# Optimization experiments

Measured on AMD Instinct MI355X. Metric: run time of the kernel, lower is better.

The kernel has to match this reference:

```python
import jax, jax.numpy as jnp
import numpy as np

N = 500_000   # total nodes across the batch of session graphs
B = 8192      # number of graphs
D = 128       # input_dim == output_dim (fc_out is None)
H = 128       # hidden_dim


def setup_inputs() -> dict:
    key = jax.random.key(0)
    ks = jax.random.split(key, 7)
    x_invar = jax.random.normal(ks[0], (N, D), jnp.float32)
    x_var = jax.random.normal(ks[1], (N, D), jnp.float32)
    s = 1.0 / np.sqrt(D)
    Wu = jax.random.normal(ks[2], (H, D), jnp.float32) * s
    bu = jnp.zeros((H,), jnp.float32)
    Wv = jax.random.normal(ks[3], (H, D), jnp.float32) * s
    We = jax.random.normal(ks[4], (1, H), jnp.float32) * (1.0 / np.sqrt(H))
    # sorted segment ids; guarantee every graph has >= 1 node
    seg_ids = jnp.sort(jnp.concatenate([
        jnp.arange(B, dtype=jnp.int32),
        jax.random.randint(ks[5], (N - B,), 0, B, dtype=jnp.int32),
    ]))
    # last node index of each graph = cumsum(counts) - 1
    counts = jax.ops.segment_sum(jnp.ones((N,), jnp.int32), seg_ids, num_segments=B)
    last_nodes = (jnp.cumsum(counts) - 1).astype(jnp.int32)
    return dict(x_invar=x_invar, x_var=x_var, Wu=Wu, bu=bu, Wv=Wv, We=We,
                seg_ids=seg_ids, last_nodes=last_nodes, num_graphs=B)


def _segment_softmax(e, seg, num_segments):
    # e: [M]; numerically stable per-segment softmax
    m = jax.ops.segment_max(e, seg, num_segments=num_segments)
    ex = jnp.exp(e - m[seg])
    den = jax.ops.segment_sum(ex, seg, num_segments=num_segments)
    return ex / den[seg]


def reference(x_invar, x_var, Wu, bu, Wv, We, seg_ids, last_nodes, num_graphs):
    # hybrid granularity, order=1: per-graph [invar; var] node rows.
    # Segment softmax/sum are permutation-invariant within a segment, so we
    # concatenate globally and double the segment ids.
    feats = jnp.concatenate([x_invar, x_var], axis=0)          # [2N, D]
    seg2 = jnp.concatenate([seg_ids, seg_ids], axis=0)         # [2N]
    feat_u = feats @ Wu.T + bu                                 # [2N, H]
    v_invar = (x_invar[last_nodes] @ Wv.T)[seg2]               # [2N, H]
    v_var = (x_var[last_nodes] @ Wv.T)[seg2]                   # [2N, H]
    e_invar = (jax.nn.sigmoid(feat_u + v_invar) @ We.T)[:, 0]  # [2N]
    e_var = (jax.nn.sigmoid(feat_u + v_var) @ We.T)[:, 0]      # [2N]
    a_invar = _segment_softmax(e_invar, seg2, num_graphs)[:, None]
    a_var = _segment_softmax(e_var, seg2, num_graphs)[:, None]
    rst_invar = jax.ops.segment_sum(feats * a_invar, seg2, num_segments=num_graphs)  # [B, D]
    rst_var = jax.ops.segment_sum(feats * a_var, seg2, num_segments=num_graphs)      # [B, D]
    return rst_invar[:, None, :], rst_var[:, None, :]          # [B, 1, D] each (order=1)
```

## Files before the change

kernel.cpp:

```cpp
#include <hip/hip_runtime.h>
#include <stdint.h>

typedef short short8 __attribute__((ext_vector_type(8)));
typedef float f32x4 __attribute__((ext_vector_type(4)));

#define D 128
#define LOG2E 1.44269504088896340736f

__device__ __forceinline__ unsigned short f2bf(float f) {
    union { float f; unsigned u; } v; v.f = f;
    unsigned u = v.u;
    unsigned r = (u + 0x7FFFu + ((u >> 16) & 1u)) >> 16;
    return (unsigned short)r;
}

__device__ __forceinline__ unsigned packbf(float x, float y) {
    unsigned ux = __float_as_uint(x) + 0x8000u;
    unsigned uy = __float_as_uint(y) + 0x8000u;
    return __builtin_amdgcn_perm(uy, ux, 0x07060302u);
}

__device__ __forceinline__ float sigm2(float z) {
    return __builtin_amdgcn_rcpf(1.f + __builtin_amdgcn_exp2f(-z));
}

__device__ __forceinline__ void gld16(const float* g, float* l) {
    __builtin_amdgcn_global_load_lds(
        (const __attribute__((address_space(1))) void*)g,
        (__attribute__((address_space(3))) void*)l, 16, 0, 0);
}

__global__ __launch_bounds__(256) void pack_wu(const float* __restrict__ Wu,
                                               short8* __restrict__ frag) {
    int tid = blockIdx.x * 256 + threadIdx.x;
    int nt = tid >> 8, kk = (tid >> 6) & 3, l = tid & 63;
    int col = nt * 16 + (l & 15);
    int kb  = kk * 32 + ((l >> 4) * 8);
    short8 o;
#pragma unroll
    for (int j = 0; j < 8; ++j) o[j] = (short)f2bf(Wu[col * D + kb + j] * LOG2E);
    frag[tid] = o;
}

__global__ __launch_bounds__(128) void gate_k(const float* __restrict__ xI,
                                              const float* __restrict__ xV,
                                              const float* __restrict__ Wv,
                                              const float* __restrict__ bu,
                                              const int* __restrict__ lastn,
                                              float* __restrict__ vIb,
                                              float* __restrict__ vVb) {
    __shared__ float xi[D], xv[D];
    int g = blockIdx.x, t = threadIdx.x;
    int r = lastn[g];
    xi[t] = xI[(size_t)r * D + t];
    xv[t] = xV[(size_t)r * D + t];
    __syncthreads();
    const float4* wr = (const float4*)(Wv + (size_t)t * D);
    const float4* a4 = (const float4*)xi;
    const float4* b4 = (const float4*)xv;
    float sI = 0.f, sV = 0.f;
#pragma unroll 8
    for (int i = 0; i < D / 4; ++i) {
        float4 w = wr[i], a = a4[i], b = b4[i];
        sI += w.x * a.x + w.y * a.y + w.z * a.z + w.w * a.w;
        sV += w.x * b.x + w.y * b.y + w.z * b.z + w.w * b.w;
    }
    float bias = bu[t];
    vIb[(size_t)g * D + t] = (sI + bias) * LOG2E;
    vVb[(size_t)g * D + t] = (sV + bias) * LOG2E;
}

__global__ __launch_bounds__(256) void attn_main(
    const float* __restrict__ xI, const float* __restrict__ xV,
    const float* __restrict__ We, const int* __restrict__ lastn,
    const float* __restrict__ vIb, const float* __restrict__ vVb,
    const short8* __restrict__ fragG, float* __restrict__ out, int B) {
    __shared__ short8 bfrag[2048];
    __shared__ __align__(16) float rbuf[4][2048];
    __shared__ float gl[3][D];
    __shared__ float cmbA[2][4][D];
    __shared__ float cmbM[2][4], cmbL[2][4];

    int t = threadIdx.x, lane = t & 63, w = t >> 6;
    int g = blockIdx.x;

    {
        const uint4* srcf = (const uint4*)fragG;
        uint4* dst = (uint4*)bfrag;
#pragma unroll
        for (int i = 0; i < 8; ++i) dst[i * 256 + t] = srcf[i * 256 + t];
    }
    if (t < D) {
        gl[0][t] = We[t] * LOG2E;
        gl[1][t] = vIb[(size_t)g * D + t];
        gl[2][t] = vVb[(size_t)g * D + t];
    }

    int s = (g == 0) ? 0 : (lastn[g - 1] + 1);
    int n = lastn[g] + 1 - s;

    int ch = (n + 15) >> 4;
    int total = 2 * ch;
    float* rb = &rbuf[w][0];

    auto issue = [&](int cc) {
        int hf = (cc >= ch) ? 1 : 0;
        const float* sp = hf ? xV : xI;
        int bb = (cc - hf * ch) << 4;
#pragma unroll
        for (int i = 0; i < 8; ++i) {
            int row = (i << 1) + (lane >> 5);
            int rr = bb + row; if (rr > n - 1) rr = n - 1;
            int lu = (lane & 31) ^ (row & 7);
            gld16(sp + (size_t)(s + rr) * D + (lu << 2),
                  rb + (i << 8) + (lane << 2));
        }
    };

    if (w < total) issue(w);
    __syncthreads();

    float mI = -__builtin_inff(), mV = -__builtin_inff();
    float lIs = 0.f, lVs = 0.f;
    float aI0 = 0.f, aI1 = 0.f, aV0 = 0.f, aV1 = 0.f;

    for (int c = w; c < total; c += 4) {
        int hf = (c >= ch) ? 1 : 0;
        int base = (c - hf * ch) << 4;

        asm volatile("s_waitcnt vmcnt(0)" ::: "memory");
        __builtin_amdgcn_sched_barrier(0);

        short8 af[4];
        int arow = lane & 15;
        int sw = (arow & 7) << 4;
        const char* rbc = (const char*)rb;
#pragma unroll
        for (int kk = 0; kk < 4; ++kk) {
            int byte = (arow << 9) + ((lane >> 4) << 5) + (kk << 7);
            float4 f0 = *(const float4*)(rbc + (byte ^ sw));
            float4 f1 = *(const float4*)(rbc + ((byte + 16) ^ sw));
            union { unsigned u[4]; short8 s8; } cv;
            cv.u[0] = packbf(f0.x, f0.y);
            cv.u[1] = packbf(f0.z, f0.w);
            cv.u[2] = packbf(f1.x, f1.y);
            cv.u[3] = packbf(f1.z, f1.w);
            af[kk] = cv.s8;
        }
        float fr0[16], fr1[16];
#pragma unroll
        for (int r = 0; r < 16; ++r) {
            int rsw = (r & 7) << 4;
            fr0[r] = *(const float*)(rbc + (((r << 9) + (lane << 2)) ^ rsw));
            fr1[r] = *(const float*)(rbc + (((r << 9) + 256 + (lane << 2)) ^ rsw));
        }
        asm volatile("s_waitcnt lgkmcnt(0)" ::: "memory");
        __builtin_amdgcn_sched_barrier(0);
        if (c + 4 < total) issue(c + 4);

        float pI[4] = {0.f, 0.f, 0.f, 0.f}, pV[4] = {0.f, 0.f, 0.f, 0.f};
#pragma unroll
        for (int nt = 0; nt < 8; ++nt) {
            f32x4 dacc = {0.f, 0.f, 0.f, 0.f};
#pragma unroll
            for (int kk = 0; kk < 4; ++kk)
                dacc = __builtin_amdgcn_mfma_f32_16x16x32_bf16(
                    af[kk], bfrag[nt * 256 + kk * 64 + lane], dacc, 0, 0, 0);
            int col = nt * 16 + (lane & 15);
            float we = gl[0][col], vI = gl[1][col], vV = gl[2][col];
#pragma unroll
            for (int q = 0; q < 4; ++q) {
                float u = dacc[q];
                pI[q] = fmaf(we, sigm2(u + vI), pI[q]);
                pV[q] = fmaf(we, sigm2(u + vV), pV[q]);
            }
        }
#pragma unroll
        for (int q = 0; q < 4; ++q) {
#pragma unroll
            for (int off = 1; off < 16; off <<= 1) {
                pI[q] += __shfl_xor(pI[q], off);
                pV[q] += __shfl_xor(pV[q], off);
            }
            int r = ((lane >> 4) * 4) + q;
            if (base + r >= n) { pI[q] = -__builtin_inff(); pV[q] = -__builtin_inff(); }
        }
        float cmI = fmaxf(fmaxf(pI[0], pI[1]), fmaxf(pI[2], pI[3]));
        float cmV = fmaxf(fmaxf(pV[0], pV[1]), fmaxf(pV[2], pV[3]));
        cmI = fmaxf(cmI, __shfl_xor(cmI, 16)); cmI = fmaxf(cmI, __shfl_xor(cmI, 32));
        cmV = fmaxf(cmV, __shfl_xor(cmV, 16)); cmV = fmaxf(cmV, __shfl_xor(cmV, 32));

        float mnI = fmaxf(mI, cmI), mnV = fmaxf(mV, cmV);
        float scI = __builtin_amdgcn_exp2f(mI - mnI);
        float scV = __builtin_amdgcn_exp2f(mV - mnV);
        lIs *= scI; lVs *= scV;
        aI0 *= scI; aI1 *= scI; aV0 *= scV; aV1 *= scV;

        float wIq[4], wVq[4];
#pragma unroll
        for (int q = 0; q < 4; ++q) {
            wIq[q] = __builtin_amdgcn_exp2f(pI[q] - mnI);
            wVq[q] = __builtin_amdgcn_exp2f(pV[q] - mnV);
        }
        float sIq = wIq[0] + wIq[1] + wIq[2] + wIq[3];
        float sVq = wVq[0] + wVq[1] + wVq[2] + wVq[3];
        sIq += __shfl_xor(sIq, 16); sIq += __shfl_xor(sIq, 32);
        sVq += __shfl_xor(sVq, 16); sVq += __shfl_xor(sVq, 32);
        lIs += sIq; lVs += sVq;

#pragma unroll
        for (int r = 0; r < 16; ++r) {
            float wI = __shfl(wIq[r & 3], (r >> 2) << 4);
            float wV = __shfl(wVq[r & 3], (r >> 2) << 4);
            aI0 = fmaf(wI, fr0[r], aI0); aI1 = fmaf(wI, fr1[r], aI1);
            aV0 = fmaf(wV, fr0[r], aV0); aV1 = fmaf(wV, fr1[r], aV1);
        }
        mI = mnI; mV = mnV;
    }

    cmbA[0][w][lane] = aI0; cmbA[0][w][lane + 64] = aI1;
    cmbA[1][w][lane] = aV0; cmbA[1][w][lane + 64] = aV1;
    if (lane == 0) {
        cmbM[0][w] = mI; cmbL[0][w] = lIs;
        cmbM[1][w] = mV; cmbL[1][w] = lVs;
    }
    __syncthreads();
    {
        int st = t >> 7, d = t & 127;
        float M = fmaxf(fmaxf(cmbM[st][0], cmbM[st][1]),
                        fmaxf(cmbM[st][2], cmbM[st][3]));
        float Ls = 0.f, A = 0.f;
#pragma unroll
        for (int ww = 0; ww < 4; ++ww) {
            float e = __builtin_amdgcn_exp2f(cmbM[st][ww] - M);
            Ls += cmbL[st][ww] * e;
            A  += cmbA[st][ww][d] * e;
        }
        out[(size_t)st * B * D + (size_t)g * D + d] = A * __builtin_amdgcn_rcpf(Ls);
    }
}

extern "C" void kernel_launch(void* const* d_in, const int* in_sizes, int n_in,
                              void* d_out, int out_size, void* d_ws, size_t ws_size,
                              hipStream_t stream) {
    const float* xI    = (const float*)d_in[0];
    const float* xV    = (const float*)d_in[1];
    const float* Wu    = (const float*)d_in[2];
    const float* bu    = (const float*)d_in[3];
    const float* Wv    = (const float*)d_in[4];
    const float* We    = (const float*)d_in[5];
    const int*   lastn = (const int*)d_in[7];
    const int B = in_sizes[7];

    float*  vIb   = (float*)d_ws;
    float*  vVb   = vIb + (size_t)B * D;
    short8* fragW = (short8*)(vVb + (size_t)B * D);

    pack_wu<<<8, 256, 0, stream>>>(Wu, fragW);
    gate_k<<<B, 128, 0, stream>>>(xI, xV, Wv, bu, lastn, vIb, vVb);
    attn_main<<<B, 256, 0, stream>>>(xI, xV, We, lastn, vIb, vVb, fragW,
                                     (float*)d_out, B);
}
```

Before: 271.0 us.

## Factor sigmoid exp, stream Wu fragments from global, batch gate GEMV, DPP reductions

The sigmoid is refactored as 1/(1+exp(-u)*exp(-v)). The per-graph exp(-v) factor is precomputed in the gate kernel, so the inner loop needs one exp per element shared by the invar and var branches instead of two. The gate kernel now processes 16 graphs per block with 256 threads, reusing Wv rows across 4 graphs at a time. The main kernel drops the LDS copy of Wu fragments and the gate vectors: it double-buffers fragments from global into registers, keeps We/c values in registers, and removes the initial __syncthreads. It also precomputes LDS offsets, adds a fast path for full chunks, replaces shuffle reductions with DPP adds, and moves the next prefetch issue into the MFMA loop. Risks are higher register pressure, global/L2 traffic for fragments, and exp overflow for large negative pre-activations.

```diff
diff --git a/kernel.cpp b/kernel.cpp
--- a/kernel.cpp
+++ b/kernel.cpp
@@ -20,8 +20,17 @@
     return __builtin_amdgcn_perm(uy, ux, 0x07060302u);
 }
 
-__device__ __forceinline__ float sigm2(float z) {
-    return __builtin_amdgcn_rcpf(1.f + __builtin_amdgcn_exp2f(-z));
+template <int C>
+__device__ __forceinline__ float dpp_add(float x) {
+    int y = __builtin_amdgcn_update_dpp(0, __float_as_int(x), C, 0xF, 0xF, true);
+    return x + __int_as_float(y);
+}
+__device__ __forceinline__ float red16(float x) {
+    x = dpp_add<0xB1>(x);
+    x = dpp_add<0x4E>(x);
+    x = dpp_add<0x141>(x);
+    x = dpp_add<0x140>(x);
+    return x;
 }
 
 __device__ __forceinline__ void gld16(const float* g, float* l) {
@@ -42,83 +51,114 @@
     frag[tid] = o;
 }
 
-__global__ __launch_bounds__(128) void gate_k(const float* __restrict__ xI,
+__global__ __launch_bounds__(256) void gate_k(const float* __restrict__ xI,
                                               const float* __restrict__ xV,
                                               const float* __restrict__ Wv,
                                               const float* __restrict__ bu,
                                               const int* __restrict__ lastn,
-                                              float* __restrict__ vIb,
-                                              float* __restrict__ vVb) {
-    __shared__ float xi[D], xv[D];
-    int g = blockIdx.x, t = threadIdx.x;
-    int r = lastn[g];
-    xi[t] = xI[(size_t)r * D + t];
-    xv[t] = xV[(size_t)r * D + t];
-    __syncthreads();
-    const float4* wr = (const float4*)(Wv + (size_t)t * D);
-    const float4* a4 = (const float4*)xi;
-    const float4* b4 = (const float4*)xv;
-    float sI = 0.f, sV = 0.f;
-#pragma unroll 8
-    for (int i = 0; i < D / 4; ++i) {
-        float4 w = wr[i], a = a4[i], b = b4[i];
-        sI += w.x * a.x + w.y * a.y + w.z * a.z + w.w * a.w;
-        sV += w.x * b.x + w.y * b.y + w.z * b.z + w.w * b.w;
-    }
-    float bias = bu[t];
-    vIb[(size_t)g * D + t] = (sI + bias) * LOG2E;
-    vVb[(size_t)g * D + t] = (sV + bias) * LOG2E;
+                                              float* __restrict__ cIb,
+                                              float* __restrict__ cVb, int B) {
+    __shared__ __align__(16) float xs[4][2][D];
+    int t = threadIdx.x, h = t & 127, st = t >> 7;
+    float bias = bu[h];
+    const float4* wv4 = (const float4*)(Wv + (size_t)h * D);
+    const float* src = st ? xV : xI;
+    float* dst = st ? cVb : cIb;
+    int g0 = blockIdx.x * 16;
+    for (int p = 0; p < 4; ++p) {
+        int gb = g0 + p * 4;
+#pragma unroll
+        for (int j = 0; j < 4; ++j) {
+            int gg = gb + j; if (gg >= B) gg = B - 1;
+            xs[j][st][h] = src[(size_t)lastn[gg] * D + h];
+        }
+        __syncthreads();
+        const float4* x0 = (const float4*)xs[0][st];
+        const float4* x1 = (const float4*)xs[1][st];
+        const float4* x2 = (const float4*)xs[2][st];
+        const float4* x3 = (const float4*)xs[3][st];
+        float a0 = 0.f, a1 = 0.f, a2 = 0.f, a3 = 0.f;
+#pragma unroll
+        for (int i = 0; i < 32; ++i) {
+            float4 w = wv4[i], b;
+            b = x0[i]; a0 += w.x*b.x + w.y*b.y + w.z*b.z + w.w*b.w;
+            b = x1[i]; a1 += w.x*b.x + w.y*b.y + w.z*b.z + w.w*b.w;
+            b = x2[i]; a2 += w.x*b.x + w.y*b.y + w.z*b.z + w.w*b.w;
+            b = x3[i]; a3 += w.x*b.x + w.y*b.y + w.z*b.z + w.w*b.w;
+        }
+        if (gb + 0 < B) dst[(size_t)(gb+0)*D + h] = __builtin_amdgcn_exp2f(-(a0+bias)*LOG2E);
+        if (gb + 1 < B) dst[(size_t)(gb+1)*D + h] = __builtin_amdgcn_exp2f(-(a1+bias)*LOG2E);
+        if (gb + 2 < B) dst[(size_t)(gb+2)*D + h] = __builtin_amdgcn_exp2f(-(a2+bias)*LOG2E);
+        if (gb + 3 < B) dst[(size_t)(gb+3)*D + h] = __builtin_amdgcn_exp2f(-(a3+bias)*LOG2E);
+        __syncthreads();
+    }
 }
 
 __global__ __launch_bounds__(256) void attn_main(
     const float* __restrict__ xI, const float* __restrict__ xV,
     const float* __restrict__ We, const int* __restrict__ lastn,
-    const float* __restrict__ vIb, const float* __restrict__ vVb,
+    const float* __restrict__ cIb, const float* __restrict__ cVb,
     const short8* __restrict__ fragG, float* __restrict__ out, int B) {
-    __shared__ short8 bfrag[2048];
     __shared__ __align__(16) float rbuf[4][2048];
-    __shared__ float gl[3][D];
     __shared__ float cmbA[2][4][D];
     __shared__ float cmbM[2][4], cmbL[2][4];
 
     int t = threadIdx.x, lane = t & 63, w = t >> 6;
     int g = blockIdx.x;
 
-    {
-        const uint4* srcf = (const uint4*)fragG;
-        uint4* dst = (uint4*)bfrag;
-#pragma unroll
-        for (int i = 0; i < 8; ++i) dst[i * 256 + t] = srcf[i * 256 + t];
-    }
-    if (t < D) {
-        gl[0][t] = We[t] * LOG2E;
-        gl[1][t] = vIb[(size_t)g * D + t];
-        gl[2][t] = vVb[(size_t)g * D + t];
-    }
-
     int s = (g == 0) ? 0 : (lastn[g - 1] + 1);
     int n = lastn[g] + 1 - s;
+
+    float WeR[8], cIr[8], cVr[8];
+#pragma unroll
+    for (int nt = 0; nt < 8; ++nt) {
+        int col = nt * 16 + (lane & 15);
+        WeR[nt] = We[col] * LOG2E;
+        cIr[nt] = cIb[(size_t)g * D + col];
+        cVr[nt] = cVb[(size_t)g * D + col];
+    }
 
     int ch = (n + 15) >> 4;
     int total = 2 * ch;
     float* rb = &rbuf[w][0];
+    const char* rbc = (const char*)rb;
+
+    int loff[8];
+#pragma unroll
+    for (int i = 0; i < 8; ++i) {
+        int row = (i << 1) + (lane >> 5);
+        loff[i] = (row << 7) + (((lane & 31) ^ (row & 7)) << 2);
+    }
+    int arow = lane & 15;
+    int sw = (arow & 7) << 4;
+    int ab0 = ((arow << 9) + ((lane >> 4) << 5)) ^ sw;
+    int ab1 = ((arow << 9) + ((lane >> 4) << 5) + 16) ^ sw;
+    int frb[8];
+#pragma unroll
+    for (int j = 0; j < 8; ++j) frb[j] = (lane << 2) ^ (j << 4);
 
     auto issue = [&](int cc) {
         int hf = (cc >= ch) ? 1 : 0;
         const float* sp = hf ? xV : xI;
         int bb = (cc - hf * ch) << 4;
-#pragma unroll
-        for (int i = 0; i < 8; ++i) {
-            int row = (i << 1) + (lane >> 5);
-            int rr = bb + row; if (rr > n - 1) rr = n - 1;
-            int lu = (lane & 31) ^ (row & 7);
-            gld16(sp + (size_t)(s + rr) * D + (lu << 2),
-                  rb + (i << 8) + (lane << 2));
+        if (bb + 16 <= n) {
+            const float* pb = sp + ((size_t)(s + bb) << 7);
+#pragma unroll
+            for (int i = 0; i < 8; ++i)
+                gld16(pb + loff[i], rb + (i << 8) + (lane << 2));
+        } else {
+#pragma unroll
+            for (int i = 0; i < 8; ++i) {
+                int row = (i << 1) + (lane >> 5);
+                int rr = bb + row; if (rr > n - 1) rr = n - 1;
+                int lu = (lane & 31) ^ (row & 7);
+                gld16(sp + (size_t)(s + rr) * D + (lu << 2),
+                      rb + (i << 8) + (lane << 2));
+            }
         }
     };
 
     if (w < total) issue(w);
-    __syncthreads();
 
     float mI = -__builtin_inff(), mV = -__builtin_inff();
     float lIs = 0.f, lVs = 0.f;
@@ -132,14 +172,10 @@
         __builtin_amdgcn_sched_barrier(0);
 
         short8 af[4];
-        int arow = lane & 15;
-        int sw = (arow & 7) << 4;
-        const char* rbc = (const char*)rb;
 #pragma unroll
         for (int kk = 0; kk < 4; ++kk) {
-            int byte = (arow << 9) + ((lane >> 4) << 5) + (kk << 7);
-            float4 f0 = *(const float4*)(rbc + (byte ^ sw));
-            float4 f1 = *(const float4*)(rbc + ((byte + 16) ^ sw));
+            float4 f0 = *(const float4*)(rbc + ab0 + (kk << 7));
+            float4 f1 = *(const float4*)(rbc + ab1 + (kk << 7));
             union { unsigned u[4]; short8 s8; } cv;
             cv.u[0] = packbf(f0.x, f0.y);
             cv.u[1] = packbf(f0.z, f0.w);
@@ -150,40 +186,48 @@
         float fr0[16], fr1[16];
 #pragma unroll
         for (int r = 0; r < 16; ++r) {
-            int rsw = (r & 7) << 4;
-            fr0[r] = *(const float*)(rbc + (((r << 9) + (lane << 2)) ^ rsw));
-            fr1[r] = *(const float*)(rbc + (((r << 9) + 256 + (lane << 2)) ^ rsw));
+            const char* p = rbc + frb[r & 7] + (r << 9);
+            fr0[r] = *(const float*)p;
+            fr1[r] = *(const float*)(p + 256);
         }
         asm volatile("s_waitcnt lgkmcnt(0)" ::: "memory");
         __builtin_amdgcn_sched_barrier(0);
-        if (c + 4 < total) issue(c + 4);
 
         float pI[4] = {0.f, 0.f, 0.f, 0.f}, pV[4] = {0.f, 0.f, 0.f, 0.f};
+        short8 bf[2][4];
+#pragma unroll
+        for (int kk = 0; kk < 4; ++kk) bf[0][kk] = fragG[(kk << 6) + lane];
 #pragma unroll
         for (int nt = 0; nt < 8; ++nt) {
+            if (nt < 7) {
+#pragma unroll
+                for (int kk = 0; kk < 4; ++kk)
+                    bf[(nt + 1) & 1][kk] = fragG[(nt + 1) * 256 + (kk << 6) + lane];
+            } else if (c + 4 < total) {
+                issue(c + 4);
+            }
             f32x4 dacc = {0.f, 0.f, 0.f, 0.f};
 #pragma unroll
             for (int kk = 0; kk < 4; ++kk)
                 dacc = __builtin_amdgcn_mfma_f32_16x16x32_bf16(
-                    af[kk], bfrag[nt * 256 + kk * 64 + lane], dacc, 0, 0, 0);
-            int col = nt * 16 + (lane & 15);
-            float we = gl[0][col], vI = gl[1][col], vV = gl[2][col];
+                    af[kk], bf[nt & 1][kk], dacc, 0, 0, 0);
 #pragma unroll
             for (int q = 0; q < 4; ++q) {
-                float u = dacc[q];
-                pI[q] = fmaf(we, sigm2(u + vI), pI[q]);
-                pV[q] = fmaf(we, sigm2(u + vV), pV[q]);
+                float tt = __builtin_amdgcn_exp2f(-dacc[q]);
+                float dI = fmaf(tt, cIr[nt], 1.f);
+                float dV = fmaf(tt, cVr[nt], 1.f);
+                pI[q] = fmaf(WeR[nt], __builtin_amdgcn_rcpf(dI), pI[q]);
+                pV[q] = fmaf(WeR[nt], __builtin_amdgcn_rcpf(dV), pV[q]);
             }
         }
 #pragma unroll
-        for (int q = 0; q < 4; ++q) {
-#pragma unroll
-            for (int off = 1; off < 16; off <<= 1) {
-                pI[q] += __shfl_xor(pI[q], off);
-                pV[q] += __shfl_xor(pV[q], off);
+        for (int q = 0; q < 4; ++q) { pI[q] = red16(pI[q]); pV[q] = red16(pV[q]); }
+        if (base + 16 > n) {
+#pragma unroll
+            for (int q = 0; q < 4; ++q) {
+                int r = ((lane >> 4) << 2) + q;
+                if (base + r >= n) { pI[q] = -__builtin_inff(); pV[q] = -__builtin_inff(); }
             }
-            int r = ((lane >> 4) * 4) + q;
-            if (base + r >= n) { pI[q] = -__builtin_inff(); pV[q] = -__builtin_inff(); }
         }
         float cmI = fmaxf(fmaxf(pI[0], pI[1]), fmaxf(pI[2], pI[3]));
         float cmV = fmaxf(fmaxf(pV[0], pV[1]), fmaxf(pV[2], pV[3]));
@@ -252,12 +296,12 @@
     const int*   lastn = (const int*)d_in[7];
     const int B = in_sizes[7];
 
-    float*  vIb   = (float*)d_ws;
-    float*  vVb   = vIb + (size_t)B * D;
-    short8* fragW = (short8*)(vVb + (size_t)B * D);
+    float*  cIb   = (float*)d_ws;
+    float*  cVb   = cIb + (size_t)B * D;
+    short8* fragW = (short8*)(cVb + (size_t)B * D);
 
     pack_wu<<<8, 256, 0, stream>>>(Wu, fragW);
-    gate_k<<<B, 128, 0, stream>>>(xI, xV, Wv, bu, lastn, vIb, vVb);
-    attn_main<<<B, 256, 0, stream>>>(xI, xV, We, lastn, vIb, vVb, fragW,
+    gate_k<<<(B + 15) / 16, 256, 0, stream>>>(xI, xV, Wv, bu, lastn, cIb, cVb, B);
+    attn_main<<<B, 256, 0, stream>>>(xI, xV, We, lastn, cIb, cVb, fragW,
                                      (float*)d_out, B);
 }
```

Result: slower. 335.7 us (+23.9%).
